# Kernel optimization log

Hardware: AMD Instinct MI355X
Metric: run time of the kernel (lower is better)

Reference implementation:

```python
import jax, jax.numpy as jnp
import numpy as np

TAU = 2.0          # LIFNode tau
ALPHA = 2.0        # spikingjelly ATan surrogate alpha (default)
EPS = 1e-5         # nn.LayerNorm eps
SCALE = 0.125      # qk_scale
NUM_HEADS = 2

@jax.custom_vjp
def spike(x):
    # heaviside(x >= 0) with ATan surrogate gradient
    return (x >= 0.0).astype(x.dtype)

def _spike_fwd(x):
    return spike(x), x

def _spike_bwd(x, g):
    sg = (ALPHA / 2.0) / (1.0 + (jnp.pi / 2.0 * ALPHA * x) ** 2)
    return (g * sg,)

spike.defvjp(_spike_fwd, _spike_bwd)

def lif(x, v_th):
    # LIFNode(tau=2.0, decay_input=True, v_reset=0.0, detach_reset=True)
    # x: [T, ...]; sequential membrane-potential scan over T
    def step(v, xt):
        v = v + (xt - v) / TAU                      # charge with input decay
        s = spike(v - v_th)                          # fire
        v = v * (1.0 - jax.lax.stop_gradient(s))     # hard reset to 0, detached
        return v, s
    _, s = jax.lax.scan(step, jnp.zeros_like(x[0]), x)
    return s

def ln(x, w, b):
    m = x.mean(-1, keepdims=True)
    var = x.var(-1, keepdims=True)
    return (x - m) / jnp.sqrt(var + EPS) * w + b

def setup_inputs() -> dict:
    key = jax.random.key(0)
    ks = jax.random.split(key, 6)
    T, B, L, H = 4, 64, 200, 256
    x = jax.random.normal(ks[0], (T, B, L, H), dtype=jnp.float32)
    std = 0.05
    qw = jax.random.normal(ks[1], (H, H), dtype=jnp.float32) * std
    kw = jax.random.normal(ks[2], (H, H), dtype=jnp.float32) * std
    vw = jax.random.normal(ks[3], (H, H), dtype=jnp.float32) * std
    pw = jax.random.normal(ks[4], (H, H), dtype=jnp.float32) * std
    pb = jnp.zeros((H,), dtype=jnp.float32)
    ones = jnp.ones((H,), dtype=jnp.float32)
    zeros = jnp.zeros((H,), dtype=jnp.float32)
    return {
        'x': x,
        'qw': qw, 'q_ln_w': ones, 'q_ln_b': zeros,
        'kw': kw, 'k_ln_w': ones, 'k_ln_b': zeros,
        'vw': vw, 'v_ln_w': ones, 'v_ln_b': zeros,
        'pw': pw, 'pb': pb, 'p_ln_w': ones, 'p_ln_b': zeros,
    }

def reference(x, qw, q_ln_w, q_ln_b, kw, k_ln_w, k_ln_b, vw, v_ln_w, v_ln_b, pw, pb, p_ln_w, p_ln_b):
    T, B, L, H = x.shape
    nh = NUM_HEADS
    dh = H // nh

    def branch(w, lw, lb):
        y = ln(x @ w.T, lw, lb)           # Linear (no bias) -> LayerNorm
        y = lif(y, 1.0)                   # LIF spikes in {0,1}
        return y.reshape(T, B, L, nh, dh).transpose(0, 1, 3, 2, 4)  # [T,B,h,L,dh]

    q = branch(qw, q_ln_w, q_ln_b)
    k = branch(kw, k_ln_w, k_ln_b)
    v = branch(vw, v_ln_w, v_ln_b)

    attn = jnp.einsum('tbhld,tbhmd->tbhlm', q, k) * SCALE   # [T,B,h,L,L]
    y = jnp.einsum('tbhlm,tbhmd->tbhld', attn, v)            # [T,B,h,L,dh]
    y = y.transpose(0, 1, 3, 2, 4).reshape(T, B, L, H)
    y = lif(y, 0.5)                                          # attn_lif, v_threshold=0.5
    y = ln(y @ pw.T + pb, p_ln_w, p_ln_b)                    # proj Linear (bias) -> LN
    return lif(y, 1.0)                                       # proj_lif
```

## Files before the change

### kernel.cpp

```cpp
#include <hip/hip_runtime.h>

#define T_ 4
#define B_ 64
#define L_ 200
#define H_ 256
#define NH_ 2
#define DH_ 128
#define LCAP 12800

typedef short short8_t __attribute__((ext_vector_type(8)));
typedef float f32x4 __attribute__((ext_vector_type(4)));

#define MFMA_BF16(a, b, c) __builtin_amdgcn_mfma_f32_16x16x32_bf16((a), (b), (c), 0, 0, 0)

__device__ __forceinline__ unsigned short bf16rn(float f) {
  unsigned u = __float_as_uint(f);
  return (unsigned short)((u + 0x7FFFu + ((u >> 16) & 1u)) >> 16);
}
__device__ __forceinline__ float bf16tof(unsigned short h) {
  return __uint_as_float(((unsigned)h) << 16);
}

__device__ __forceinline__ short8_t unpack_bf16(uint2 v) {
  union { short8_t s; unsigned u[4]; } r;
  r.u[0] = __builtin_amdgcn_perm(0u, v.x, 0x0C010C00u) * 0x3F80u;
  r.u[1] = __builtin_amdgcn_perm(0u, v.x, 0x0C030C02u) * 0x3F80u;
  r.u[2] = __builtin_amdgcn_perm(0u, v.y, 0x0C010C00u) * 0x3F80u;
  r.u[3] = __builtin_amdgcn_perm(0u, v.y, 0x0C030C02u) * 0x3F80u;
  return r.s;
}

__global__ void pack_w(const float* __restrict__ qw, const float* __restrict__ kw,
                       const float* __restrict__ vw, const float* __restrict__ pw,
                       short* __restrict__ wf, float* __restrict__ wT) {
  int id = blockIdx.x * 256 + threadIdx.x;
  if (id < 262144) {
    int mat = id >> 16, k = (id >> 8) & 255, j = id & 255;
    const float* src = (mat == 0) ? qw : (mat == 1) ? kw : (mat == 2) ? vw : pw;
    wT[id] = src[j * 256 + k];
  }
  int fid = id - 262144;
  if (fid >= 0 && fid < 98304) {
    int lane = fid & 63, kc = (fid >> 6) & 7, nt = (fid >> 9) & 15, ms = fid >> 13;
    int mat = ms / 3, s = ms - mat * 3;
    const float* src = (mat == 0) ? qw : (mat == 1) ? kw : (mat == 2) ? vw : pw;
    int n = nt * 16 + (lane & 15), q = lane >> 4;
    for (int j = 0; j < 8; j++) {
      float v = src[n * 256 + kc * 32 + q * 8 + j];
      unsigned short h1 = bf16rn(v);
      float r1 = v - bf16tof(h1);
      unsigned short h2 = bf16rn(r1);
      float r2 = r1 - bf16tof(h2);
      unsigned short h3 = bf16rn(r2);
      wf[fid * 8 + j] = (short)((s == 0) ? h1 : (s == 1) ? h2 : h3);
    }
  }
}

__global__ void zero_cnt(int* __restrict__ cnt) {
  if (threadIdx.x < 4) cnt[threadIdx.x] = 0;
}

#define LOAD_A_QKV(kc, aa0, aa1)                                         \
  do {                                                                   \
    int ap_ = (lane ^ (kc)) * 8;                                         \
    aa0[0] = *(const short8_t*)&sa[(kc) * 512 + ap_];                    \
    aa0[1] = *(const short8_t*)&sa[(8 + (kc)) * 512 + ap_];              \
    aa1[0] = *(const short8_t*)&sa[8192 + (kc) * 512 + ap_];             \
    aa1[1] = *(const short8_t*)&sa[8192 + (8 + (kc)) * 512 + ap_];       \
  } while (0)

#define QKV_STEP(aa0, aa1, b0a, b1a)                                     \
  do {                                                                   \
    _Pragma("unroll")                                                    \
    for (int jj_ = 0; jj_ < 4; jj_++)                                    \
      _Pragma("unroll")                                                  \
      for (int mt_ = 0; mt_ < 2; mt_++)                                  \
        hi[mt_][jj_] = MFMA_BF16(aa0[mt_], b0a[jj_], hi[mt_][jj_]);      \
    _Pragma("unroll")                                                    \
    for (int jj_ = 0; jj_ < 4; jj_++)                                    \
      _Pragma("unroll")                                                  \
      for (int mt_ = 0; mt_ < 2; mt_++)                                  \
        lo[mt_][jj_] = MFMA_BF16(aa0[mt_], b1a[jj_], lo[mt_][jj_]);      \
    _Pragma("unroll")                                                    \
    for (int jj_ = 0; jj_ < 4; jj_++)                                    \
      _Pragma("unroll")                                                  \
      for (int mt_ = 0; mt_ < 2; mt_++)                                  \
        lo[mt_][jj_] = MFMA_BF16(aa1[mt_], b0a[jj_], lo[mt_][jj_]);      \
  } while (0)

__global__ __launch_bounds__(256, 2)
void gemm_qkv(const float* __restrict__ xf, const short* __restrict__ wf,
              const float* __restrict__ qlnw, const float* __restrict__ qlnb,
              const float* __restrict__ klnw, const float* __restrict__ klnb,
              const float* __restrict__ vlnw, const float* __restrict__ vlnb,
              unsigned char* __restrict__ Qsp, unsigned char* __restrict__ Ksp,
              unsigned char* __restrict__ Vsp,
              int* __restrict__ cnt, int* __restrict__ list) {
  __shared__ short sa[2 * 8192];
  __shared__ float reds[3][32][4];
  __shared__ float redq[3][32][4];
  __shared__ int pf[24];
  const int tid = threadIdx.x;
  const int w = tid >> 6, lane = tid & 63;
  const int q = lane >> 4, ln = lane & 15;
  const int p0 = blockIdx.x * 8;
  const int jbase = w * 4;

  if (tid < 24) pf[tid] = 0;

  short8_t bA0[4], bA1[4], bB0[4], bB1[4];
  short8_t aC0[2], aC1[2], aN0[2], aN1[2];
#pragma unroll
  for (int jj = 0; jj < 4; jj++) {
    const short* bp = wf + (size_t)(jbase + jj) * 4096 + lane * 8;
    bA0[jj] = *(const short8_t*)bp;
    bA1[jj] = *(const short8_t*)(bp + 65536);
  }

  for (int it = 0; it < 4; it++) {
    int cid = tid + 256 * it;
    int r = cid >> 5, ck = cid & 31;
    int k0 = ck * 8, kc = ck >> 2, cq = ck & 3;
    int mt = r >> 4, m = r & 15;
    int p = r >> 2, t = r & 3;
    int pi = p0 + p;
    int b = pi / L_, l = pi % L_;
    size_t nrow = ((size_t)t * B_ + b) * L_ + l;
    int base = ((mt * 8 + kc) * 512) + (((cq * 16 + m) ^ (kc & 7)) * 8);
    float4 v0 = *(const float4*)(xf + nrow * H_ + k0);
    float4 v1 = *(const float4*)(xf + nrow * H_ + k0 + 4);
    float f[8] = {v0.x, v0.y, v0.z, v0.w, v1.x, v1.y, v1.z, v1.w};
    union { short8_t v; short s[8]; } H1, H2;
#pragma unroll
    for (int e = 0; e < 8; e++) {
      unsigned short h1 = bf16rn(f[e]);
      float r1 = f[e] - bf16tof(h1);
      unsigned short h2 = bf16rn(r1);
      H1.s[e] = (short)h1; H2.s[e] = (short)h2;
    }
    *(short8_t*)&sa[base] = H1.v;
    *(short8_t*)&sa[base + 8192] = H2.v;
  }
  __syncthreads();

  LOAD_A_QKV(0, aC0, aC1);

  for (int mat = 0; mat < 3; mat++) {
    const float* lnw = (mat == 0) ? qlnw : (mat == 1) ? klnw : vlnw;
    const float* lnb = (mat == 0) ? qlnb : (mat == 1) ? klnb : vlnb;
    unsigned char* spk = (mat == 0) ? Qsp : (mat == 1) ? Ksp : Vsp;
    const short* wb = wf + (size_t)mat * 196608;

    f32x4 hi[2][4], lo[2][4];
#pragma unroll
    for (int mt = 0; mt < 2; mt++)
#pragma unroll
      for (int jj = 0; jj < 4; jj++) {
        f32x4 z = {0.f, 0.f, 0.f, 0.f};
        hi[mt][jj] = z; lo[mt][jj] = z;
      }

#pragma unroll
    for (int kh = 0; kh < 4; kh++) {
      const int kc = 2 * kh;
#pragma unroll
      for (int jj = 0; jj < 4; jj++) {
        const short* bp = wb + (size_t)(kc + 1) * 512 + (size_t)(jbase + jj) * 4096 + lane * 8;
        bB0[jj] = *(const short8_t*)bp;
        bB1[jj] = *(const short8_t*)(bp + 65536);
      }
      LOAD_A_QKV(kc + 1, aN0, aN1);
      QKV_STEP(aC0, aC1, bA0, bA1);
      {
        const short* nx = (kc + 2 < 8) ? (wb + (size_t)(kc + 2) * 512) : (wb + 196608);
#pragma unroll
        for (int jj = 0; jj < 4; jj++) {
          const short* bp = nx + (size_t)(jbase + jj) * 4096 + lane * 8;
          bA0[jj] = *(const short8_t*)bp;
          bA1[jj] = *(const short8_t*)(bp + 65536);
        }
      }
      LOAD_A_QKV((kc + 2) & 7, aC0, aC1);
      QKV_STEP(aN0, aN1, bB0, bB1);
    }

    float y[2][4][4];
#pragma unroll
    for (int mt = 0; mt < 2; mt++)
#pragma unroll
      for (int jj = 0; jj < 4; jj++)
#pragma unroll
        for (int i = 0; i < 4; i++)
          y[mt][jj][i] = hi[mt][jj][i] + lo[mt][jj][i];

#pragma unroll
    for (int mt = 0; mt < 2; mt++)
#pragma unroll
      for (int i = 0; i < 4; i++) {
        float s = y[mt][0][i] + y[mt][1][i] + y[mt][2][i] + y[mt][3][i];
        float ss = y[mt][0][i] * y[mt][0][i] + y[mt][1][i] * y[mt][1][i]
                 + y[mt][2][i] * y[mt][2][i] + y[mt][3][i] * y[mt][3][i];
#pragma unroll
        for (int o = 1; o < 16; o <<= 1) {
          s += __shfl_xor(s, o, 64);
          ss += __shfl_xor(ss, o, 64);
        }
        if (ln == 0) { reds[mat][16 * mt + 4 * q + i][w] = s; redq[mat][16 * mt + 4 * q + i][w] = ss; }
      }
    __syncthreads();
    float m_[2][4], rs_[2][4], tolr[2][4];
#pragma unroll
    for (int mt = 0; mt < 2; mt++)
#pragma unroll
      for (int i = 0; i < 4; i++) {
        int r = 16 * mt + 4 * q + i;
        float S = reds[mat][r][0] + reds[mat][r][1] + reds[mat][r][2] + reds[mat][r][3];
        float Q2 = redq[mat][r][0] + redq[mat][r][1] + redq[mat][r][2] + redq[mat][r][3];
        float mm = S * (1.0f / 256.0f);
        float var = Q2 * (1.0f / 256.0f) - mm * mm;
        float rs = 1.0f / sqrtf(var + 1e-5f);
        m_[mt][i] = mm; rs_[mt][i] = rs;
        tolr[mt][i] = 1.75e-4f + 3e-6f * (4.0f + fabsf(mm) * rs);
      }

    int fl[2] = {0, 0};
#pragma unroll
    for (int mt = 0; mt < 2; mt++) {
      int pi = p0 + 4 * mt + q;
      int b = pi / L_, l = pi % L_;
#pragma unroll
      for (int jj = 0; jj < 4; jj++) {
        int col = (w * 4 + jj) * 16 + ln;
        float lw = lnw[col], lb = lnb[col];
        float v = 0.0f;
#pragma unroll
        for (int t = 0; t < 4; t++) {
          float yn = (y[mt][jj][t] - m_[mt][t]) * rs_[mt][t] * lw + lb;
          v = (v + yn) * 0.5f;
          bool f = (v >= 1.0f);
          if (fabsf(v - 1.0f) < tolr[mt][t]) fl[mt] = 1;
          int head = col >> 7, d = col & 127;
          spk[((((size_t)t * B_ + b) * NH_ + head) * L_ + l) * DH_ + d] = f ? (unsigned char)1 : (unsigned char)0;
          if (f) v = 0.0f;
        }
      }
    }
#pragma unroll
    for (int o = 1; o < 16; o <<= 1) {
      fl[0] |= __shfl_xor(fl[0], o, 64);
      fl[1] |= __shfl_xor(fl[1], o, 64);
    }
    if (ln == 0) {
      if (fl[0]) atomicOr(&pf[mat * 8 + q], 1);
      if (fl[1]) atomicOr(&pf[mat * 8 + 4 + q], 1);
    }
  }

  __syncthreads();
  if (tid < 24 && pf[tid]) {
    int mat = tid >> 3, pr = tid & 7;
    int idx = atomicAdd(cnt + mat, 1);
    if (idx < LCAP) list[mat * LCAP + idx] = p0 + pr;
  }
}

#define LOAD_A_PROJ(kc, aa)                                              \
  do {                                                                   \
    int ap_ = (lane ^ (kc)) * 8;                                         \
    aa[0] = *(const short8_t*)&sa[(kc) * 512 + ap_];                     \
    aa[1] = *(const short8_t*)&sa[(8 + (kc)) * 512 + ap_];               \
  } while (0)

#define PROJ_STEP(aa, b0a, b1a)                                          \
  do {                                                                   \
    _Pragma("unroll")                                                    \
    for (int jj_ = 0; jj_ < 4; jj_++)                                    \
      _Pragma("unroll")                                                  \
      for (int mt_ = 0; mt_ < 2; mt_++)                                  \
        hi[mt_][jj_] = MFMA_BF16(aa[mt_], b0a[jj_], hi[mt_][jj_]);       \
    _Pragma("unroll")                                                    \
    for (int jj_ = 0; jj_ < 4; jj_++)                                    \
      _Pragma("unroll")                                                  \
      for (int mt_ = 0; mt_ < 2; mt_++)                                  \
        lo[mt_][jj_] = MFMA_BF16(aa[mt_], b1a[jj_], lo[mt_][jj_]);       \
  } while (0)

__global__ __launch_bounds__(256, 2)
void gemm_proj(const unsigned char* __restrict__ xs, const short* __restrict__ wfm,
               const float* __restrict__ bias,
               const float* __restrict__ lnw, const float* __restrict__ lnb,
               float* __restrict__ out,
               int* __restrict__ cnt, int* __restrict__ list) {
  __shared__ short sa[8192];
  __shared__ float reds[32][4];
  __shared__ float redq[32][4];
  __shared__ int pf[8];
  const int tid = threadIdx.x;
  const int w = tid >> 6, lane = tid & 63;
  const int q = lane >> 4, ln = lane & 15;
  const int p0 = blockIdx.x * 8;
  const int jbase = w * 4;

  if (tid < 8) pf[tid] = 0;

  short8_t bA0[4], bA1[4], bB0[4], bB1[4];
  short8_t aC[2], aN[2];
#pragma unroll
  for (int jj = 0; jj < 4; jj++) {
    const short* bp = wfm + (size_t)(jbase + jj) * 4096 + lane * 8;
    bA0[jj] = *(const short8_t*)bp;
    bA1[jj] = *(const short8_t*)(bp + 65536);
  }

  for (int it = 0; it < 4; it++) {
    int cid = tid + 256 * it;
    int r = cid >> 5, ck = cid & 31;
    int k0 = ck * 8, kc = ck >> 2, cq = ck & 3;
    int mt = r >> 4, m = r & 15;
    int p = r >> 2, t = r & 3;
    int pi = p0 + p;
    int b = pi / L_, l = pi % L_;
    size_t nrow = ((size_t)t * B_ + b) * L_ + l;
    int base = ((mt * 8 + kc) * 512) + (((cq * 16 + m) ^ (kc & 7)) * 8);
    uint2 u = *(const uint2*)(xs + nrow * H_ + k0);
    *(short8_t*)&sa[base] = unpack_bf16(u);
  }
  __syncthreads();

  f32x4 hi[2][4], lo[2][4];
#pragma unroll
  for (int mt = 0; mt < 2; mt++)
#pragma unroll
    for (int jj = 0; jj < 4; jj++) {
      f32x4 z = {0.f, 0.f, 0.f, 0.f};
      hi[mt][jj] = z; lo[mt][jj] = z;
    }

  LOAD_A_PROJ(0, aC);

#pragma unroll
  for (int kh = 0; kh < 4; kh++) {
    const int kc = 2 * kh;
#pragma unroll
    for (int jj = 0; jj < 4; jj++) {
      const short* bp = wfm + (size_t)(kc + 1) * 512 + (size_t)(jbase + jj) * 4096 + lane * 8;
      bB0[jj] = *(const short8_t*)bp;
      bB1[jj] = *(const short8_t*)(bp + 65536);
    }
    LOAD_A_PROJ(kc + 1, aN);
    PROJ_STEP(aC, bA0, bA1);
    if (kc + 2 < 8) {
#pragma unroll
      for (int jj = 0; jj < 4; jj++) {
        const short* bp = wfm + (size_t)(kc + 2) * 512 + (size_t)(jbase + jj) * 4096 + lane * 8;
        bA0[jj] = *(const short8_t*)bp;
        bA1[jj] = *(const short8_t*)(bp + 65536);
      }
      LOAD_A_PROJ(kc + 2, aC);
    }
    PROJ_STEP(aN, bB0, bB1);
  }

  float y[2][4][4];
#pragma unroll
  for (int mt = 0; mt < 2; mt++)
#pragma unroll
    for (int jj = 0; jj < 4; jj++) {
      float bj = bias[(w * 4 + jj) * 16 + ln];
#pragma unroll
      for (int i = 0; i < 4; i++)
        y[mt][jj][i] = hi[mt][jj][i] + lo[mt][jj][i] + bj;
    }

#pragma unroll
  for (int mt = 0; mt < 2; mt++)
#pragma unroll
    for (int i = 0; i < 4; i++) {
      float s = y[mt][0][i] + y[mt][1][i] + y[mt][2][i] + y[mt][3][i];
      float ss = y[mt][0][i] * y[mt][0][i] + y[mt][1][i] * y[mt][1][i]
               + y[mt][2][i] * y[mt][2][i] + y[mt][3][i] * y[mt][3][i];
#pragma unroll
      for (int o = 1; o < 16; o <<= 1) {
        s += __shfl_xor(s, o, 64);
        ss += __shfl_xor(ss, o, 64);
      }
      if (ln == 0) { reds[16 * mt + 4 * q + i][w] = s; redq[16 * mt + 4 * q + i][w] = ss; }
    }
  __syncthreads();
  float m_[2][4], rs_[2][4], tolr[2][4];
#pragma unroll
  for (int mt = 0; mt < 2; mt++)
#pragma unroll
    for (int i = 0; i < 4; i++) {
      int r = 16 * mt + 4 * q + i;
      float S = reds[r][0] + reds[r][1] + reds[r][2] + reds[r][3];
      float Q2 = redq[r][0] + redq[r][1] + redq[r][2] + redq[r][3];
      float mm = S * (1.0f / 256.0f);
      float var = Q2 * (1.0f / 256.0f) - mm * mm;
      float rs = 1.0f / sqrtf(var + 1e-5f);
      m_[mt][i] = mm; rs_[mt][i] = rs;
      tolr[mt][i] = 1.75e-4f + 3e-6f * (4.0f + fabsf(mm) * rs);
    }

  int fl[2] = {0, 0};
#pragma unroll
  for (int mt = 0; mt < 2; mt++) {
    int pi = p0 + 4 * mt + q;
    int b = pi / L_, l = pi % L_;
#pragma unroll
    for (int jj = 0; jj < 4; jj++) {
      int col = (w * 4 + jj) * 16 + ln;
      float lw = lnw[col], lb = lnb[col];
      float v = 0.0f;
#pragma unroll
      for (int t = 0; t < 4; t++) {
        float yn = (y[mt][jj][t] - m_[mt][t]) * rs_[mt][t] * lw + lb;
        v = (v + yn) * 0.5f;
        bool f = (v >= 1.0f);
        if (fabsf(v - 1.0f) < tolr[mt][t]) fl[mt] = 1;
        size_t n = ((size_t)t * B_ + b) * L_ + l;
        out[n * H_ + col] = f ? 1.0f : 0.0f;
        if (f) v = 0.0f;
      }
    }
  }
#pragma unroll
  for (int o = 1; o < 16; o <<= 1) {
    fl[0] |= __shfl_xor(fl[0], o, 64);
    fl[1] |= __shfl_xor(fl[1], o, 64);
  }
  if (ln == 0) {
    if (fl[0]) atomicOr(&pf[q], 1);
    if (fl[1]) atomicOr(&pf[4 + q], 1);
  }
  __syncthreads();
  if (tid < 8 && pf[tid]) {
    int idx = atomicAdd(cnt, 1);
    if (idx < LCAP) list[idx] = p0 + tid;
  }
}

__global__ __launch_bounds__(256)
void fixup_qkv(const float* __restrict__ xf, const float* __restrict__ wT,
               const float* __restrict__ qlnw, const float* __restrict__ qlnb,
               const float* __restrict__ klnw, const float* __restrict__ klnb,
               const float* __restrict__ vlnw, const float* __restrict__ vlnb,
               unsigned char* __restrict__ Qsp, unsigned char* __restrict__ Ksp,
               unsigned char* __restrict__ Vsp,
               const int* __restrict__ cnt, const int* __restrict__ list) {
  __shared__ float sx[4][256];
  __shared__ double rsum[4][4];
  __shared__ double mv[4], rsd[4];
  const int tid = threadIdx.x;
  const int w = tid >> 6, lane = tid & 63;
  int n0 = cnt[0]; if (n0 > LCAP) n0 = LCAP;
  int n1 = cnt[1]; if (n1 > LCAP) n1 = LCAP;
  int n2 = cnt[2]; if (n2 > LCAP) n2 = LCAP;
  int ntot = n0 + n1 + n2;
  for (int e = blockIdx.x; e < ntot; e += gridDim.x) {
    int mat, ei;
    if (e < n0) { mat = 0; ei = e; }
    else if (e < n0 + n1) { mat = 1; ei = e - n0; }
    else { mat = 2; ei = e - n0 - n1; }
    const float* wTm = wT + (size_t)mat * 65536;
    const float* lnw = (mat == 0) ? qlnw : (mat == 1) ? klnw : vlnw;
    const float* lnb = (mat == 0) ? qlnb : (mat == 1) ? klnb : vlnb;
    unsigned char* spk = (mat == 0) ? Qsp : (mat == 1) ? Ksp : Vsp;
    int pi = list[mat * LCAP + ei];
    int b = pi / L_, l = pi % L_;

    {
      size_t nrow = ((size_t)w * B_ + b) * L_ + l;
      float4 v = *(const float4*)(xf + nrow * H_ + lane * 4);
      *(float4*)&sx[w][lane * 4] = v;
    }
    __syncthreads();

    double acc[4] = {0.0, 0.0, 0.0, 0.0};
    for (int k = 0; k < 256; k++) {
      double wv = (double)wTm[k * 256 + tid];
      acc[0] += (double)sx[0][k] * wv;
      acc[1] += (double)sx[1][k] * wv;
      acc[2] += (double)sx[2][k] * wv;
      acc[3] += (double)sx[3][k] * wv;
    }
#pragma unroll
    for (int t = 0; t < 4; t++) {
      double s = acc[t];
#pragma unroll
      for (int o = 1; o < 64; o <<= 1) s += __shfl_xor(s, o, 64);
      if (lane == 0) rsum[w][t] = s;
    }
    __syncthreads();
    if (tid < 4) mv[tid] = (rsum[0][tid] + rsum[1][tid] + rsum[2][tid] + rsum[3][tid]) * (1.0 / 256.0);
    __syncthreads();
#pragma unroll
    for (int t = 0; t < 4; t++) {
      double d = acc[t] - mv[t];
      double ss = d * d;
#pragma unroll
      for (int o = 1; o < 64; o <<= 1) ss += __shfl_xor(ss, o, 64);
      if (lane == 0) rsum[w][t] = ss;
    }
    __syncthreads();
    if (tid < 4) {
      double var = (rsum[0][tid] + rsum[1][tid] + rsum[2][tid] + rsum[3][tid]) * (1.0 / 256.0);
      rsd[tid] = 1.0 / sqrt(var + 1e-5);
    }
    __syncthreads();
    double lw = (double)lnw[tid], lb = (double)lnb[tid];
    int head = tid >> 7, d = tid & 127;
    double v = 0.0;
#pragma unroll
    for (int t = 0; t < 4; t++) {
      double yn = (acc[t] - mv[t]) * rsd[t] * lw + lb;
      v = (v + yn) * 0.5;
      bool f = (v >= 1.0);
      spk[((((size_t)t * B_ + b) * NH_ + head) * L_ + l) * DH_ + d] = f ? (unsigned char)1 : (unsigned char)0;
      if (f) v = 0.0;
    }
    __syncthreads();
  }
}

__global__ __launch_bounds__(256)
void fixup_proj(const unsigned char* __restrict__ xs, const float* __restrict__ wT,
                const float* __restrict__ bias,
                const float* __restrict__ lnw, const float* __restrict__ lnb,
                float* __restrict__ out,
                const int* __restrict__ cnt, const int* __restrict__ list) {
  __shared__ float sx[4][256];
  __shared__ double rsum[4][4];
  __shared__ double mv[4], rsd[4];
  const int tid = threadIdx.x;
  const int w = tid >> 6, lane = tid & 63;
  int n = *cnt; if (n > LCAP) n = LCAP;
  for (int e = blockIdx.x; e < n; e += gridDim.x) {
    int pi = list[e];
    int b = pi / L_, l = pi % L_;
    size_t nrowW = ((size_t)w * B_ + b) * L_ + l;

    {
      uchar4 u = *(const uchar4*)(xs + nrowW * H_ + lane * 4);
      float4 v = make_float4((float)u.x, (float)u.y, (float)u.z, (float)u.w);
      *(float4*)&sx[w][lane * 4] = v;
    }
    __syncthreads();

    double acc[4];
    double bj = (double)bias[tid];
#pragma unroll
    for (int t = 0; t < 4; t++) acc[t] = bj;
    for (int k = 0; k < 256; k++) {
      double wv = (double)wT[k * 256 + tid];
      acc[0] += (double)sx[0][k] * wv;
      acc[1] += (double)sx[1][k] * wv;
      acc[2] += (double)sx[2][k] * wv;
      acc[3] += (double)sx[3][k] * wv;
    }
#pragma unroll
    for (int t = 0; t < 4; t++) {
      double s = acc[t];
#pragma unroll
      for (int o = 1; o < 64; o <<= 1) s += __shfl_xor(s, o, 64);
      if (lane == 0) rsum[w][t] = s;
    }
    __syncthreads();
    if (tid < 4) mv[tid] = (rsum[0][tid] + rsum[1][tid] + rsum[2][tid] + rsum[3][tid]) * (1.0 / 256.0);
    __syncthreads();
#pragma unroll
    for (int t = 0; t < 4; t++) {
      double d = acc[t] - mv[t];
      double ss = d * d;
#pragma unroll
      for (int o = 1; o < 64; o <<= 1) ss += __shfl_xor(ss, o, 64);
      if (lane == 0) rsum[w][t] = ss;
    }
    __syncthreads();
    if (tid < 4) {
      double var = (rsum[0][tid] + rsum[1][tid] + rsum[2][tid] + rsum[3][tid]) * (1.0 / 256.0);
      rsd[tid] = 1.0 / sqrt(var + 1e-5);
    }
    __syncthreads();
    double lw = (double)lnw[tid], lb = (double)lnb[tid];
    double v = 0.0;
#pragma unroll
    for (int t = 0; t < 4; t++) {
      double yn = (acc[t] - mv[t]) * rsd[t] * lw + lb;
      v = (v + yn) * 0.5;
      bool f = (v >= 1.0);
      out[(((size_t)t * B_ + b) * L_ + l) * H_ + tid] = f ? 1.0f : 0.0f;
      if (f) v = 0.0;
    }
    __syncthreads();
  }
}

__global__ __launch_bounds__(256)
void vt_prep(const unsigned char* __restrict__ Vs, unsigned char* __restrict__ Vt) {
  const int slab = blockIdx.x;
  const int w = threadIdx.x >> 6, lane = threadIdx.x & 63;
  const unsigned char* src = Vs + (size_t)slab * (L_ * DH_);
  unsigned char* dst = Vt + (size_t)slab * (DH_ * 224);
  for (int d = w; d < DH_; d += 4) {
    for (int mb = 0; mb < 4; mb++) {
      int m = mb * 64 + lane;
      unsigned char v = 0;
      if (m < L_) v = src[(size_t)m * DH_ + d];
      if (m < 224) dst[(size_t)d * 224 + m] = v;
    }
  }
}

__global__ __launch_bounds__(256)
void attn_mfma(const unsigned char* __restrict__ Qs, const unsigned char* __restrict__ Ks,
               const unsigned char* __restrict__ Vt, unsigned char* __restrict__ S2) {
  __shared__ unsigned short sS[32 * 232];
  const int tid = threadIdx.x;
  const int w = tid >> 6, lane = tid & 63;
  const int quad = lane >> 4, ln = lane & 15;
  const int bid = blockIdx.x;
  const int lt = bid % 7;
  const int head = (bid / 7) & 1;
  const int b = bid / 14;
  const int l0 = lt * 32;

  for (int i = tid; i < 32 * 232; i += 256) sS[i] = 0;

  float vmem[2][2][4];
#pragma unroll
  for (int di = 0; di < 2; di++)
#pragma unroll
    for (int ls = 0; ls < 2; ls++)
#pragma unroll
      for (int r = 0; r < 4; r++) vmem[di][ls][r] = 0.f;

  __syncthreads();

  for (int t = 0; t < T_; t++) {
    const int slab = (t * B_ + b) * NH_ + head;
    const unsigned char* qb = Qs + (size_t)slab * (L_ * DH_) + (size_t)l0 * DH_;
    const unsigned char* kb = Ks + (size_t)slab * (L_ * DH_);

    short8_t af[2][4];
#pragma unroll
    for (int ls = 0; ls < 2; ls++)
#pragma unroll
      for (int ks = 0; ks < 4; ks++)
        af[ls][ks] = unpack_bf16(*(const uint2*)(qb + (size_t)(ls * 16 + ln) * DH_ + ks * 32 + quad * 8));

#pragma unroll
    for (int i = 0; i < 4; i++) {
      int nt = w + 4 * i;
      if (nt < 13) {
        short8_t bf[4];
#pragma unroll
        for (int ks = 0; ks < 4; ks++)
          bf[ks] = unpack_bf16(*(const uint2*)(kb + (size_t)(nt * 16 + ln) * DH_ + ks * 32 + quad * 8));
#pragma unroll
        for (int ls = 0; ls < 2; ls++) {
          f32x4 acc = {0.f, 0.f, 0.f, 0.f};
#pragma unroll
          for (int ks = 0; ks < 4; ks++)
            acc = MFMA_BF16(af[ls][ks], bf[ks], acc);
#pragma unroll
          for (int r = 0; r < 4; r++)
            sS[(ls * 16 + quad * 4 + r) * 232 + nt * 16 + ln] =
                (unsigned short)(__float_as_uint(acc[r]) >> 16);
        }
      }
    }
    __syncthreads();

    const unsigned char* vb = Vt + (size_t)slab * (DH_ * 224);
    f32x4 a2[2][2];
#pragma unroll
    for (int di = 0; di < 2; di++)
#pragma unroll
      for (int ls = 0; ls < 2; ls++) { f32x4 z = {0.f, 0.f, 0.f, 0.f}; a2[di][ls] = z; }

#pragma unroll
    for (int ks = 0; ks < 7; ks++) {
      short8_t s0 = *(const short8_t*)&sS[(0 * 16 + ln) * 232 + ks * 32 + quad * 8];
      short8_t s1 = *(const short8_t*)&sS[(1 * 16 + ln) * 232 + ks * 32 + quad * 8];
#pragma unroll
      for (int di = 0; di < 2; di++) {
        int dt = w + 4 * di;
        short8_t bv = unpack_bf16(*(const uint2*)(vb + (size_t)(dt * 16 + ln) * 224 + ks * 32 + quad * 8));
        a2[di][0] = MFMA_BF16(s0, bv, a2[di][0]);
        a2[di][1] = MFMA_BF16(s1, bv, a2[di][1]);
      }
    }

#pragma unroll
    for (int di = 0; di < 2; di++)
#pragma unroll
      for (int ls = 0; ls < 2; ls++)
#pragma unroll
        for (int r = 0; r < 4; r++) {
          float y = a2[di][ls][r] * 0.125f;
          float v = (vmem[di][ls][r] + y) * 0.5f;
          bool f = (v >= 0.5f);
          int l = l0 + ls * 16 + quad * 4 + r;
          if (l < L_)
            S2[(((size_t)t * B_ + b) * L_ + l) * H_ + head * DH_ + (w + 4 * di) * 16 + ln] =
                f ? (unsigned char)1 : (unsigned char)0;
          vmem[di][ls][r] = f ? 0.f : v;
        }
    __syncthreads();
  }
}

extern "C" void kernel_launch(void* const* d_in, const int* in_sizes, int n_in,
                              void* d_out, int out_size, void* d_ws, size_t ws_size,
                              hipStream_t stream) {
  (void)in_sizes; (void)n_in; (void)out_size; (void)ws_size;
  const float* x    = (const float*)d_in[0];
  const float* qw   = (const float*)d_in[1];
  const float* qlnw = (const float*)d_in[2];
  const float* qlnb = (const float*)d_in[3];
  const float* kw   = (const float*)d_in[4];
  const float* klnw = (const float*)d_in[5];
  const float* klnb = (const float*)d_in[6];
  const float* vw   = (const float*)d_in[7];
  const float* vlnw = (const float*)d_in[8];
  const float* vlnb = (const float*)d_in[9];
  const float* pw   = (const float*)d_in[10];
  const float* pb   = (const float*)d_in[11];
  const float* plnw = (const float*)d_in[12];
  const float* plnb = (const float*)d_in[13];

  char* ws = (char*)d_ws;
  const size_t SPK = (size_t)T_ * B_ * NH_ * L_ * DH_;
  short* wf  = (short*)ws;
  float* wT  = (float*)(ws + 1572864);
  int*  cnt  = (int*)(ws + 2621440);
  int*  list = (int*)(ws + 2621696);
  unsigned char* Qsp = (unsigned char*)(ws + 2826496);
  unsigned char* Ksp = Qsp + SPK;
  unsigned char* Vsp = Ksp + SPK;
  unsigned char* S2  = Vsp;
  unsigned char* Vt  = Vsp + SPK;

  hipLaunchKernelGGL(pack_w, dim3(1408), dim3(256), 0, stream, qw, kw, vw, pw, wf, wT);
  hipLaunchKernelGGL(zero_cnt, dim3(1), dim3(64), 0, stream, cnt);

  hipLaunchKernelGGL(gemm_qkv, dim3(1600), dim3(256), 0, stream,
                     x, wf, qlnw, qlnb, klnw, klnb, vlnw, vlnb, Qsp, Ksp, Vsp, cnt, list);

  hipLaunchKernelGGL(fixup_qkv, dim3(2048), dim3(256), 0, stream,
                     x, wT, qlnw, qlnb, klnw, klnb, vlnw, vlnb, Qsp, Ksp, Vsp, cnt, list);

  hipLaunchKernelGGL(vt_prep, dim3(512), dim3(256), 0, stream, Vsp, Vt);
  hipLaunchKernelGGL(attn_mfma, dim3(896), dim3(256), 0, stream, Qsp, Ksp, Vt, S2);

  hipLaunchKernelGGL(gemm_proj, dim3(1600), dim3(256), 0, stream,
                     S2, wf + 589824, pb, plnw, plnb, (float*)d_out, cnt + 3, list + 3 * LCAP);
  hipLaunchKernelGGL(fixup_proj, dim3(2048), dim3(256), 0, stream,
                     S2, wT + 196608, pb, plnw, plnb, (float*)d_out, cnt + 3, list + 3 * LCAP);
}
```

Before: 435.5 us.

## Halve QKV GEMM block tile to raise occupancy, drop register double-buffering

The fused QKV GEMM+LayerNorm+LIF kernel now handles 4 positions (16 rows) per block instead of 8, launching twice as many blocks with half the shared memory. Launch bounds go from 2 to 4 blocks per SM, and the explicit A/B register double-buffering and prefetch pipeline is replaced by a simple per-kc loop. The aim is more resident waves to hide latency and lower register pressure. The cost is that each weight fragment loaded from global memory now feeds half as many MFMAs, so weight traffic per output doubles and the prefetch overlap is lost.

```diff
diff --git a/kernel.cpp b/kernel.cpp
--- a/kernel.cpp
+++ b/kernel.cpp
@@ -61,35 +61,7 @@
   if (threadIdx.x < 4) cnt[threadIdx.x] = 0;
 }
 
-#define LOAD_A_QKV(kc, aa0, aa1)                                         \
-  do {                                                                   \
-    int ap_ = (lane ^ (kc)) * 8;                                         \
-    aa0[0] = *(const short8_t*)&sa[(kc) * 512 + ap_];                    \
-    aa0[1] = *(const short8_t*)&sa[(8 + (kc)) * 512 + ap_];              \
-    aa1[0] = *(const short8_t*)&sa[8192 + (kc) * 512 + ap_];             \
-    aa1[1] = *(const short8_t*)&sa[8192 + (8 + (kc)) * 512 + ap_];       \
-  } while (0)
-
-#define QKV_STEP(aa0, aa1, b0a, b1a)                                     \
-  do {                                                                   \
-    _Pragma("unroll")                                                    \
-    for (int jj_ = 0; jj_ < 4; jj_++)                                    \
-      _Pragma("unroll")                                                  \
-      for (int mt_ = 0; mt_ < 2; mt_++)                                  \
-        hi[mt_][jj_] = MFMA_BF16(aa0[mt_], b0a[jj_], hi[mt_][jj_]);      \
-    _Pragma("unroll")                                                    \
-    for (int jj_ = 0; jj_ < 4; jj_++)                                    \
-      _Pragma("unroll")                                                  \
-      for (int mt_ = 0; mt_ < 2; mt_++)                                  \
-        lo[mt_][jj_] = MFMA_BF16(aa0[mt_], b1a[jj_], lo[mt_][jj_]);      \
-    _Pragma("unroll")                                                    \
-    for (int jj_ = 0; jj_ < 4; jj_++)                                    \
-      _Pragma("unroll")                                                  \
-      for (int mt_ = 0; mt_ < 2; mt_++)                                  \
-        lo[mt_][jj_] = MFMA_BF16(aa1[mt_], b0a[jj_], lo[mt_][jj_]);      \
-  } while (0)
-
-__global__ __launch_bounds__(256, 2)
+__global__ __launch_bounds__(256, 4)
 void gemm_qkv(const float* __restrict__ xf, const short* __restrict__ wf,
               const float* __restrict__ qlnw, const float* __restrict__ qlnb,
               const float* __restrict__ klnw, const float* __restrict__ klnb,
@@ -97,37 +69,27 @@
               unsigned char* __restrict__ Qsp, unsigned char* __restrict__ Ksp,
               unsigned char* __restrict__ Vsp,
               int* __restrict__ cnt, int* __restrict__ list) {
-  __shared__ short sa[2 * 8192];
-  __shared__ float reds[3][32][4];
-  __shared__ float redq[3][32][4];
-  __shared__ int pf[24];
+  __shared__ short sa[2 * 4096];
+  __shared__ float reds[3][16][4];
+  __shared__ float redq[3][16][4];
+  __shared__ int pf[12];
   const int tid = threadIdx.x;
   const int w = tid >> 6, lane = tid & 63;
   const int q = lane >> 4, ln = lane & 15;
-  const int p0 = blockIdx.x * 8;
+  const int p0 = blockIdx.x * 4;
   const int jbase = w * 4;
 
-  if (tid < 24) pf[tid] = 0;
-
-  short8_t bA0[4], bA1[4], bB0[4], bB1[4];
-  short8_t aC0[2], aC1[2], aN0[2], aN1[2];
-#pragma unroll
-  for (int jj = 0; jj < 4; jj++) {
-    const short* bp = wf + (size_t)(jbase + jj) * 4096 + lane * 8;
-    bA0[jj] = *(const short8_t*)bp;
-    bA1[jj] = *(const short8_t*)(bp + 65536);
-  }
-
-  for (int it = 0; it < 4; it++) {
+  if (tid < 12) pf[tid] = 0;
+
+  for (int it = 0; it < 2; it++) {
     int cid = tid + 256 * it;
     int r = cid >> 5, ck = cid & 31;
     int k0 = ck * 8, kc = ck >> 2, cq = ck & 3;
-    int mt = r >> 4, m = r & 15;
     int p = r >> 2, t = r & 3;
     int pi = p0 + p;
     int b = pi / L_, l = pi % L_;
     size_t nrow = ((size_t)t * B_ + b) * L_ + l;
-    int base = ((mt * 8 + kc) * 512) + (((cq * 16 + m) ^ (kc & 7)) * 8);
+    int base = (kc * 512) + (((cq * 16 + r) ^ (kc & 7)) * 8);
     float4 v0 = *(const float4*)(xf + nrow * H_ + k0);
     float4 v1 = *(const float4*)(xf + nrow * H_ + k0 + 4);
     float f[8] = {v0.x, v0.y, v0.z, v0.w, v1.x, v1.y, v1.z, v1.w};
@@ -140,11 +102,9 @@
       H1.s[e] = (short)h1; H2.s[e] = (short)h2;
     }
     *(short8_t*)&sa[base] = H1.v;
-    *(short8_t*)&sa[base + 8192] = H2.v;
+    *(short8_t*)&sa[base + 4096] = H2.v;
   }
   __syncthreads();
-
-  LOAD_A_QKV(0, aC0, aC1);
 
   for (int mat = 0; mat < 3; mat++) {
     const float* lnw = (mat == 0) ? qlnw : (mat == 1) ? klnw : vlnw;
@@ -152,82 +112,71 @@
     unsigned char* spk = (mat == 0) ? Qsp : (mat == 1) ? Ksp : Vsp;
     const short* wb = wf + (size_t)mat * 196608;
 
-    f32x4 hi[2][4], lo[2][4];
-#pragma unroll
-    for (int mt = 0; mt < 2; mt++)
+    f32x4 hi[4], lo[4];
+#pragma unroll
+    for (int jj = 0; jj < 4; jj++) {
+      f32x4 z = {0.f, 0.f, 0.f, 0.f};
+      hi[jj] = z; lo[jj] = z;
+    }
+
+    for (int kc = 0; kc < 8; kc++) {
+      short8_t b0[4], b1[4];
 #pragma unroll
       for (int jj = 0; jj < 4; jj++) {
-        f32x4 z = {0.f, 0.f, 0.f, 0.f};
-        hi[mt][jj] = z; lo[mt][jj] = z;
+        const short* bp = wb + (size_t)kc * 512 + (size_t)(jbase + jj) * 4096 + lane * 8;
+        b0[jj] = *(const short8_t*)bp;
+        b1[jj] = *(const short8_t*)(bp + 65536);
       }
-
-#pragma unroll
-    for (int kh = 0; kh < 4; kh++) {
-      const int kc = 2 * kh;
-#pragma unroll
-      for (int jj = 0; jj < 4; jj++) {
-        const short* bp = wb + (size_t)(kc + 1) * 512 + (size_t)(jbase + jj) * 4096 + lane * 8;
-        bB0[jj] = *(const short8_t*)bp;
-        bB1[jj] = *(const short8_t*)(bp + 65536);
+      int ap = (lane ^ kc) * 8;
+      short8_t a0 = *(const short8_t*)&sa[kc * 512 + ap];
+      short8_t a1 = *(const short8_t*)&sa[4096 + kc * 512 + ap];
+#pragma unroll
+      for (int jj = 0; jj < 4; jj++)
+        hi[jj] = MFMA_BF16(a0, b0[jj], hi[jj]);
+#pragma unroll
+      for (int jj = 0; jj < 4; jj++)
+        lo[jj] = MFMA_BF16(a0, b1[jj], lo[jj]);
+#pragma unroll
+      for (int jj = 0; jj < 4; jj++)
+        lo[jj] = MFMA_BF16(a1, b0[jj], lo[jj]);
+    }
+
+    float y[4][4];
+#pragma unroll
+    for (int jj = 0; jj < 4; jj++)
+#pragma unroll
+      for (int i = 0; i < 4; i++)
+        y[jj][i] = hi[jj][i] + lo[jj][i];
+
+#pragma unroll
+    for (int i = 0; i < 4; i++) {
+      float s = y[0][i] + y[1][i] + y[2][i] + y[3][i];
+      float ss = y[0][i] * y[0][i] + y[1][i] * y[1][i]
+               + y[2][i] * y[2][i] + y[3][i] * y[3][i];
+#pragma unroll
+      for (int o = 1; o < 16; o <<= 1) {
+        s += __shfl_xor(s, o, 64);
+        ss += __shfl_xor(ss, o, 64);
       }
-      LOAD_A_QKV(kc + 1, aN0, aN1);
-      QKV_STEP(aC0, aC1, bA0, bA1);
-      {
-        const short* nx = (kc + 2 < 8) ? (wb + (size_t)(kc + 2) * 512) : (wb + 196608);
-#pragma unroll
-        for (int jj = 0; jj < 4; jj++) {
-          const short* bp = nx + (size_t)(jbase + jj) * 4096 + lane * 8;
-          bA0[jj] = *(const short8_t*)bp;
-          bA1[jj] = *(const short8_t*)(bp + 65536);
-        }
-      }
-      LOAD_A_QKV((kc + 2) & 7, aC0, aC1);
-      QKV_STEP(aN0, aN1, bB0, bB1);
-    }
-
-    float y[2][4][4];
-#pragma unroll
-    for (int mt = 0; mt < 2; mt++)
-#pragma unroll
-      for (int jj = 0; jj < 4; jj++)
-#pragma unroll
-        for (int i = 0; i < 4; i++)
-          y[mt][jj][i] = hi[mt][jj][i] + lo[mt][jj][i];
-
-#pragma unroll
-    for (int mt = 0; mt < 2; mt++)
-#pragma unroll
-      for (int i = 0; i < 4; i++) {
-        float s = y[mt][0][i] + y[mt][1][i] + y[mt][2][i] + y[mt][3][i];
-        float ss = y[mt][0][i] * y[mt][0][i] + y[mt][1][i] * y[mt][1][i]
-                 + y[mt][2][i] * y[mt][2][i] + y[mt][3][i] * y[mt][3][i];
-#pragma unroll
-        for (int o = 1; o < 16; o <<= 1) {
-          s += __shfl_xor(s, o, 64);
-          ss += __shfl_xor(ss, o, 64);
-        }
-        if (ln == 0) { reds[mat][16 * mt + 4 * q + i][w] = s; redq[mat][16 * mt + 4 * q + i][w] = ss; }
-      }
-    __syncthreads();
-    float m_[2][4], rs_[2][4], tolr[2][4];
-#pragma unroll
-    for (int mt = 0; mt < 2; mt++)
-#pragma unroll
-      for (int i = 0; i < 4; i++) {
-        int r = 16 * mt + 4 * q + i;
-        float S = reds[mat][r][0] + reds[mat][r][1] + reds[mat][r][2] + reds[mat][r][3];
-        float Q2 = redq[mat][r][0] + redq[mat][r][1] + redq[mat][r][2] + redq[mat][r][3];
-        float mm = S * (1.0f / 256.0f);
-        float var = Q2 * (1.0f / 256.0f) - mm * mm;
-        float rs = 1.0f / sqrtf(var + 1e-5f);
-        m_[mt][i] = mm; rs_[mt][i] = rs;
-        tolr[mt][i] = 1.75e-4f + 3e-6f * (4.0f + fabsf(mm) * rs);
-      }
-
-    int fl[2] = {0, 0};
-#pragma unroll
-    for (int mt = 0; mt < 2; mt++) {
-      int pi = p0 + 4 * mt + q;
+      if (ln == 0) { reds[mat][4 * q + i][w] = s; redq[mat][4 * q + i][w] = ss; }
+    }
+    __syncthreads();
+    float m_[4], rs_[4], tolr[4];
+#pragma unroll
+    for (int i = 0; i < 4; i++) {
+      int r = 4 * q + i;
+      float S = reds[mat][r][0] + reds[mat][r][1] + reds[mat][r][2] + reds[mat][r][3];
+      float Q2 = redq[mat][r][0] + redq[mat][r][1] + redq[mat][r][2] + redq[mat][r][3];
+      float mm = S * (1.0f / 256.0f);
+      float var = Q2 * (1.0f / 256.0f) - mm * mm;
+      float rs = 1.0f / sqrtf(var + 1e-5f);
+      m_[i] = mm; rs_[i] = rs;
+      tolr[i] = 1.75e-4f + 3e-6f * (4.0f + fabsf(mm) * rs);
+    }
+
+    int fl = 0;
+    {
+      int pi = p0 + q;
       int b = pi / L_, l = pi % L_;
 #pragma unroll
       for (int jj = 0; jj < 4; jj++) {
@@ -236,10 +185,10 @@
         float v = 0.0f;
 #pragma unroll
         for (int t = 0; t < 4; t++) {
-          float yn = (y[mt][jj][t] - m_[mt][t]) * rs_[mt][t] * lw + lb;
+          float yn = (y[jj][t] - m_[t]) * rs_[t] * lw + lb;
           v = (v + yn) * 0.5f;
           bool f = (v >= 1.0f);
-          if (fabsf(v - 1.0f) < tolr[mt][t]) fl[mt] = 1;
+          if (fabsf(v - 1.0f) < tolr[t]) fl = 1;
           int head = col >> 7, d = col & 127;
           spk[((((size_t)t * B_ + b) * NH_ + head) * L_ + l) * DH_ + d] = f ? (unsigned char)1 : (unsigned char)0;
           if (f) v = 0.0f;
@@ -247,19 +196,13 @@
       }
     }
 #pragma unroll
-    for (int o = 1; o < 16; o <<= 1) {
-      fl[0] |= __shfl_xor(fl[0], o, 64);
-      fl[1] |= __shfl_xor(fl[1], o, 64);
-    }
-    if (ln == 0) {
-      if (fl[0]) atomicOr(&pf[mat * 8 + q], 1);
-      if (fl[1]) atomicOr(&pf[mat * 8 + 4 + q], 1);
-    }
+    for (int o = 1; o < 16; o <<= 1) fl |= __shfl_xor(fl, o, 64);
+    if (ln == 0 && fl) atomicOr(&pf[mat * 4 + q], 1);
   }
 
   __syncthreads();
-  if (tid < 24 && pf[tid]) {
-    int mat = tid >> 3, pr = tid & 7;
+  if (tid < 12 && pf[tid]) {
+    int mat = tid >> 2, pr = tid & 3;
     int idx = atomicAdd(cnt + mat, 1);
     if (idx < LCAP) list[mat * LCAP + idx] = p0 + pr;
   }
@@ -746,7 +689,7 @@
   hipLaunchKernelGGL(pack_w, dim3(1408), dim3(256), 0, stream, qw, kw, vw, pw, wf, wT);
   hipLaunchKernelGGL(zero_cnt, dim3(1), dim3(64), 0, stream, cnt);
 
-  hipLaunchKernelGGL(gemm_qkv, dim3(1600), dim3(256), 0, stream,
+  hipLaunchKernelGGL(gemm_qkv, dim3(3200), dim3(256), 0, stream,
                      x, wf, qlnw, qlnb, klnw, klnb, vlnw, vlnb, Qsp, Ksp, Vsp, cnt, list);
 
   hipLaunchKernelGGL(fixup_qkv, dim3(2048), dim3(256), 0, stream,
```

Result: no change. 441.3 us (+1.3%).
